# Kernel optimization log

Hardware: AMD Instinct MI355X
Metric: run time of the kernel (lower is better)

Reference implementation:

```python
import jax, jax.numpy as jnp
import numpy as np

N = 50000        # nodes
DEG = 16         # in-degree per node
E = N * DEG      # edges
IN_F, HID, NCLS = 128, 128, 64
B, L = 1024, 50  # sentence batch, sentence length


def _linear_init(key, fan_in, fan_out):
    s = 1.0 / np.sqrt(fan_in)
    kw, kb = jax.random.split(key)
    W = jax.random.uniform(kw, (fan_in, fan_out), jnp.float32, -s, s)
    b = jax.random.uniform(kb, (fan_out,), jnp.float32, -s, s)
    return W, b


def setup_inputs() -> dict:
    key = jax.random.key(0)
    ks = jax.random.split(key, 9)
    inputs = jax.random.normal(ks[0], (N, IN_F), jnp.float32)
    src = jax.random.randint(ks[1], (E,), 0, N, dtype=jnp.int32)
    # every node has exactly DEG incoming edges -> DGL recv on all nodes is well-defined
    dst = jnp.repeat(jnp.arange(N, dtype=jnp.int32), DEG)
    sentence = jax.random.randint(ks[2], (B, L), 0, N, dtype=jnp.int32)
    W1, b1 = _linear_init(ks[3], IN_F, HID)
    W2, b2 = _linear_init(ks[4], HID, NCLS)
    Wf1, bf1 = _linear_init(ks[5], NCLS, 256)
    Wf2, bf2 = _linear_init(ks[6], 256, 128)
    Wf3, bf3 = _linear_init(ks[7], 128, 2)
    return {"inputs": inputs, "W1": W1, "b1": b1, "W2": W2, "b2": b2,
            "Wf1": Wf1, "bf1": bf1, "Wf2": Wf2, "bf2": bf2, "Wf3": Wf3, "bf3": bf3,
            "src": src, "dst": dst, "sentence": sentence}


def reference(inputs, W1, b1, W2, b2, Wf1, bf1, Wf2, bf2, Wf3, bf3, src, dst, sentence):
    def mean_agg(h):
        # gather src features, segment-mean over destinations (gcn_message/gcn_reduce)
        s = jax.ops.segment_sum(h[src], dst, num_segments=N)       # [N, d]
        cnt = jax.ops.segment_sum(jnp.ones((E, 1), h.dtype), dst, num_segments=N)
        return s / jnp.maximum(cnt, 1.0)

    x = jax.nn.relu(mean_agg(inputs) @ W1 + b1)   # gc1 + relu (dropout = identity, eval mode)
    x = mean_agg(x) @ W2 + b2                      # gc2
    x = x.at[0].set(0.0)                           # x[0] = zeros
    sent_emd = jnp.sum(x[sentence], axis=1)        # [B, NCLS]
    h1 = jax.nn.relu(sent_emd @ Wf1 + bf1)
    h2 = jax.nn.relu(h1 @ Wf2 + bf2)
    return h2 @ Wf3 + bf3                          # [B, 2]
```

## Files before the change

### kernel.cpp

```cpp
#include <hip/hip_runtime.h>

#define NNODES 50000
#define DEG    16
#define NCLS   64
#define BSENT  1024
#define LSENT  50

typedef __attribute__((ext_vector_type(8))) short short8;
typedef __attribute__((ext_vector_type(4))) float f32x4;

__device__ __forceinline__ unsigned short f2bf(float f) {
    union { float f; unsigned u; } v; v.f = f;
    unsigned r = v.u + 0x7fffu + ((v.u >> 16) & 1u);
    return (unsigned short)(r >> 16);
}
__device__ __forceinline__ unsigned pack2bf(float a, float b) {
    return (unsigned)f2bf(a) | ((unsigned)f2bf(b) << 16);
}

__device__ __forceinline__ void prep_one(const float* W, unsigned short* Bp,
                                         int idx, int NOUT) {
    int j    = idx & 7;
    int lane = (idx >> 3) & 63;
    int rem  = idx >> 9;
    int ks   = rem & 3, c = rem >> 2;
    int k = ks * 32 + (lane >> 4) * 8 + j;
    int n = c * 16 + (lane & 15);
    Bp[idx] = f2bf(W[k * NOUT + n]);
}

__global__ void prep_both(const float* __restrict__ W1, unsigned short* __restrict__ B1p,
                          const float* __restrict__ W2, unsigned short* __restrict__ B2p) {
    int idx = blockIdx.x * 256 + threadIdx.x;
    if (idx < 128 * 128)                 prep_one(W1, B1p, idx, 128);
    else if (idx < 128 * 128 + 64 * 128) prep_one(W2, B2p, idx - 128 * 128, 64);
}

__global__ __launch_bounds__(256)
void gemm_mfma1(const float* __restrict__ X, const unsigned short* __restrict__ Bp,
                unsigned short* __restrict__ Y, int M) {
    __shared__ __align__(16) unsigned short As[64 * 128];
    __shared__ __align__(16) unsigned short Bs[128 * 128];
    const int tid  = threadIdx.x;
    const int wave = tid >> 6, lane = tid & 63;
    const int mbase = blockIdx.x * 64;

#pragma unroll
    for (int i = 0; i < 8; ++i) {
        int idx = tid + i * 256;
        int row = idx >> 5;
        int c4  = idx & 31;
        int grow = mbase + row;
        int w  = row >> 4;
        int ks = c4 >> 3;
        int ln = ((c4 >> 1) & 3) * 16 + (row & 15);
        int off = ((w * 4 + ks) * 64 + ln) * 8 + (c4 & 1) * 4;
        unsigned lo = 0, hi = 0;
        if (grow < M) {
            const float4 v = *(const float4*)&X[(size_t)grow * 128 + c4 * 4];
            lo = pack2bf(v.x, v.y);
            hi = pack2bf(v.z, v.w);
        }
        *(uint2*)&As[off] = make_uint2(lo, hi);
    }
#pragma unroll
    for (int i = 0; i < 8; ++i) {
        int idx = tid + i * 256;
        *(uint4*)&Bs[idx * 8] = *(const uint4*)&Bp[idx * 8];
    }
    __syncthreads();

    const short8* Af = (const short8*)As;
    const short8* Bf = (const short8*)Bs;
    short8 a[4];
#pragma unroll
    for (int ks = 0; ks < 4; ++ks) a[ks] = Af[(wave * 4 + ks) * 64 + lane];

    f32x4 acc[8] = {};
#pragma unroll
    for (int c = 0; c < 8; ++c)
#pragma unroll
        for (int ks = 0; ks < 4; ++ks)
            acc[c] = __builtin_amdgcn_mfma_f32_16x16x32_bf16(
                a[ks], Bf[(c * 4 + ks) * 64 + lane], acc[c], 0, 0, 0);

    const int col = lane & 15, rg = lane >> 4;
#pragma unroll
    for (int c = 0; c < 8; ++c)
#pragma unroll
        for (int r = 0; r < 4; ++r) {
            int grow = mbase + wave * 16 + rg * 4 + r;
            if (grow < M) Y[(size_t)grow * 128 + c * 16 + col] = f2bf(acc[c][r]);
        }
}

__global__ __launch_bounds__(256)
void agg_gemm(const unsigned short* __restrict__ Y1, const int* __restrict__ src,
              const float* __restrict__ b1, const unsigned short* __restrict__ B2p,
              unsigned short* __restrict__ Y2, int M) {
    __shared__ __align__(16) unsigned short As[64 * 128];
    __shared__ __align__(16) unsigned short Bs[64 * 128];
    __shared__ int s_idx[64 * DEG];
    const int tid  = threadIdx.x;
    const int wave = tid >> 6, lane = tid & 63;
    const int mbase = blockIdx.x * 64;

    {
        const long eb = (long)mbase * DEG;
        int e = tid;
#pragma unroll
        for (int i = 0; i < 4; ++i, e += 256)
            s_idx[e] = (eb + e < (long)NNODES * DEG) ? src[eb + e] : 0;
    }
#pragma unroll
    for (int i = 0; i < 4; ++i) {
        int idx = tid + i * 256;
        *(uint4*)&Bs[idx * 8] = *(const uint4*)&B2p[idx * 8];
    }
    __syncthreads();

    const int c8    = tid & 15;
    const int rbase = tid >> 4;
    const int ks    = c8 >> 2;
    const int lncol = (c8 & 3) * 16;
#pragma unroll
    for (int it = 0; it < 4; ++it) {
        const int row  = it * 16 + rbase;
        const int grow = mbase + row;
        float a0 = 0.f, a1 = 0.f, a2 = 0.f, a3 = 0.f;
        float a4 = 0.f, a5 = 0.f, a6 = 0.f, a7 = 0.f;
        if (grow < M) {
            const int* sp = &s_idx[row * DEG];
#pragma unroll
            for (int j = 0; j < DEG; ++j) {
                const uint4 v = *(const uint4*)&Y1[(size_t)sp[j] * 128 + c8 * 8];
                a0 += __uint_as_float(v.x << 16);
                a1 += __uint_as_float(v.x & 0xffff0000u);
                a2 += __uint_as_float(v.y << 16);
                a3 += __uint_as_float(v.y & 0xffff0000u);
                a4 += __uint_as_float(v.z << 16);
                a5 += __uint_as_float(v.z & 0xffff0000u);
                a6 += __uint_as_float(v.w << 16);
                a7 += __uint_as_float(v.w & 0xffff0000u);
            }
            const float s = 1.f / 16.f;
            const float4 bb0 = *(const float4*)&b1[c8 * 8];
            const float4 bb1 = *(const float4*)&b1[c8 * 8 + 4];
            a0 = fmaxf(a0 * s + bb0.x, 0.f);
            a1 = fmaxf(a1 * s + bb0.y, 0.f);
            a2 = fmaxf(a2 * s + bb0.z, 0.f);
            a3 = fmaxf(a3 * s + bb0.w, 0.f);
            a4 = fmaxf(a4 * s + bb1.x, 0.f);
            a5 = fmaxf(a5 * s + bb1.y, 0.f);
            a6 = fmaxf(a6 * s + bb1.z, 0.f);
            a7 = fmaxf(a7 * s + bb1.w, 0.f);
        }
        const int off = ((it * 4 + ks) * 64 + lncol + rbase) * 8;
        uint4 o;
        o.x = pack2bf(a0, a1);
        o.y = pack2bf(a2, a3);
        o.z = pack2bf(a4, a5);
        o.w = pack2bf(a6, a7);
        *(uint4*)&As[off] = o;
    }
    __syncthreads();

    const short8* Af = (const short8*)As;
    const short8* Bf = (const short8*)Bs;
    short8 a[4];
#pragma unroll
    for (int ks2 = 0; ks2 < 4; ++ks2) a[ks2] = Af[(wave * 4 + ks2) * 64 + lane];

    f32x4 acc[4] = {};
#pragma unroll
    for (int c = 0; c < 4; ++c)
#pragma unroll
        for (int ks2 = 0; ks2 < 4; ++ks2)
            acc[c] = __builtin_amdgcn_mfma_f32_16x16x32_bf16(
                a[ks2], Bf[(c * 4 + ks2) * 64 + lane], acc[c], 0, 0, 0);

    const int col = lane & 15, rg = lane >> 4;
#pragma unroll
    for (int c = 0; c < 4; ++c)
#pragma unroll
        for (int r = 0; r < 4; ++r) {
            int grow = mbase + wave * 16 + rg * 4 + r;
            if (grow < M) Y2[(size_t)grow * 64 + c * 16 + col] = f2bf(acc[c][r]);
        }
}

__global__ __launch_bounds__(256)
void agg2(const unsigned short* __restrict__ Y, const int* __restrict__ src,
          const float* __restrict__ bias, float* __restrict__ out, int M) {
    __shared__ int s_idx[32 * DEG];
    const int tid = threadIdx.x;
    const int nb = blockIdx.x * 32;
    {
        const long eb = (long)nb * DEG;
        int e = tid;
#pragma unroll
        for (int i = 0; i < 2; ++i, e += 256)
            s_idx[e] = (eb + e < (long)NNODES * DEG) ? src[eb + e] : 0;
    }
    __syncthreads();
    const int row = tid >> 3, c8 = tid & 7;
    const int n = nb + row;
    if (n >= M) return;
    const int* sp = &s_idx[row * DEG];
    float a0 = 0.f, a1 = 0.f, a2 = 0.f, a3 = 0.f;
    float a4 = 0.f, a5 = 0.f, a6 = 0.f, a7 = 0.f;
#pragma unroll
    for (int j = 0; j < DEG; ++j) {
        const uint4 v = *(const uint4*)&Y[(size_t)sp[j] * 64 + c8 * 8];
        a0 += __uint_as_float(v.x << 16);
        a1 += __uint_as_float(v.x & 0xffff0000u);
        a2 += __uint_as_float(v.y << 16);
        a3 += __uint_as_float(v.y & 0xffff0000u);
        a4 += __uint_as_float(v.z << 16);
        a5 += __uint_as_float(v.z & 0xffff0000u);
        a6 += __uint_as_float(v.w << 16);
        a7 += __uint_as_float(v.w & 0xffff0000u);
    }
    const float s = 1.f / 16.f;
    const float4 b0 = *(const float4*)&bias[c8 * 8];
    const float4 b1v = *(const float4*)&bias[c8 * 8 + 4];
    a0 = a0 * s + b0.x;  a1 = a1 * s + b0.y;
    a2 = a2 * s + b0.z;  a3 = a3 * s + b0.w;
    a4 = a4 * s + b1v.x; a5 = a5 * s + b1v.y;
    a6 = a6 * s + b1v.z; a7 = a7 * s + b1v.w;
    if (n == 0) { a0 = a1 = a2 = a3 = a4 = a5 = a6 = a7 = 0.f; }
    float* op = &out[(size_t)n * 64 + c8 * 8];
    *(float4*)op       = make_float4(a0, a1, a2, a3);
    *(float4*)(op + 4) = make_float4(a4, a5, a6, a7);
}

__global__ __launch_bounds__(256)
void head_fused(const float* __restrict__ x2, const int* __restrict__ sentence,
                const float* __restrict__ Wf1, const float* __restrict__ bf1,
                const float* __restrict__ Wf2, const float* __restrict__ bf2,
                const float* __restrict__ Wf3, const float* __restrict__ bf3,
                float* __restrict__ out) {
    __shared__ int   s_idx[8 * LSENT];
    __shared__ float sent_s[8][64];
    __shared__ float h1_s[8][256];
    __shared__ float h2_s[8][128];
    const int tid = threadIdx.x;
    const int bs = blockIdx.x * 8;

    for (int e = tid; e < 8 * LSENT; e += 256)
        s_idx[e] = sentence[bs * LSENT + e];
    __syncthreads();

    {
        const int s = tid >> 5, l32 = tid & 31;
        float c0 = 0.f, c1 = 0.f;
        const int* sp = &s_idx[s * LSENT];
#pragma unroll 5
        for (int l = 0; l < LSENT; ++l) {
            const float2 v = *(const float2*)&x2[(size_t)sp[l] * 64 + l32 * 2];
            c0 += v.x; c1 += v.y;
        }
        sent_s[s][l32 * 2 + 0] = c0;
        sent_s[s][l32 * 2 + 1] = c1;
    }
    __syncthreads();

    {
        const int s = tid >> 5, og = (tid & 31) * 8;
        float acc[8];
#pragma unroll
        for (int j = 0; j < 8; ++j) acc[j] = bf1[og + j];
        for (int k = 0; k < 64; ++k) {
            const float xk = sent_s[s][k];
            const float4 w0 = *(const float4*)&Wf1[k * 256 + og];
            const float4 w1 = *(const float4*)&Wf1[k * 256 + og + 4];
            acc[0] += xk * w0.x; acc[1] += xk * w0.y; acc[2] += xk * w0.z; acc[3] += xk * w0.w;
            acc[4] += xk * w1.x; acc[5] += xk * w1.y; acc[6] += xk * w1.z; acc[7] += xk * w1.w;
        }
#pragma unroll
        for (int j = 0; j < 8; ++j) h1_s[s][og + j] = fmaxf(acc[j], 0.f);
    }
    __syncthreads();

    {
        const int s = tid >> 5, og = (tid & 31) * 4;
        float acc[4];
#pragma unroll
        for (int j = 0; j < 4; ++j) acc[j] = bf2[og + j];
        for (int k = 0; k < 256; ++k) {
            const float xk = h1_s[s][k];
            const float4 w = *(const float4*)&Wf2[k * 128 + og];
            acc[0] += xk * w.x; acc[1] += xk * w.y; acc[2] += xk * w.z; acc[3] += xk * w.w;
        }
#pragma unroll
        for (int j = 0; j < 4; ++j) h2_s[s][og + j] = fmaxf(acc[j], 0.f);
    }
    __syncthreads();

    if (tid < 16) {
        const int s = tid >> 1, c = tid & 1;
        float acc = bf3[c];
        for (int k = 0; k < 128; ++k)
            acc += h2_s[s][k] * Wf3[k * 2 + c];
        out[(bs + s) * 2 + c] = acc;
    }
}

extern "C" void kernel_launch(void* const* d_in, const int* in_sizes, int n_in,
                              void* d_out, int out_size, void* d_ws, size_t ws_size,
                              hipStream_t stream) {
    const float* inputs  = (const float*)d_in[0];
    const float* W1      = (const float*)d_in[1];
    const float* b1      = (const float*)d_in[2];
    const float* W2      = (const float*)d_in[3];
    const float* b2      = (const float*)d_in[4];
    const float* Wf1     = (const float*)d_in[5];
    const float* bf1     = (const float*)d_in[6];
    const float* Wf2     = (const float*)d_in[7];
    const float* bf2     = (const float*)d_in[8];
    const float* Wf3     = (const float*)d_in[9];
    const float* bf3     = (const float*)d_in[10];
    const int*   src     = (const int*)d_in[11];
    const int*   sentence= (const int*)d_in[13];
    float* out = (float*)d_out;

    char* ws = (char*)d_ws;
    size_t o = 0;
    auto alloc = [&](size_t bytes) -> char* {
        char* p = ws + o; o += (bytes + 255) & ~(size_t)255; return p;
    };
    unsigned short* Y1  = (unsigned short*)alloc((size_t)NNODES * 128 * 2);
    unsigned short* Y2  = (unsigned short*)alloc((size_t)NNODES * 64 * 2);
    float*          x2  = (float*)alloc((size_t)NNODES * 64 * 4);
    unsigned short* B1p = (unsigned short*)alloc(128 * 128 * 2);
    unsigned short* B2p = (unsigned short*)alloc(64 * 128 * 2);

    const int gridM = (NNODES + 63) / 64;

    prep_both<<<(128 * 128 + 64 * 128 + 255) / 256, 256, 0, stream>>>(W1, B1p, W2, B2p);
    gemm_mfma1<<<gridM, 256, 0, stream>>>(inputs, B1p, Y1, NNODES);
    agg_gemm<<<gridM, 256, 0, stream>>>(Y1, src, b1, B2p, Y2, NNODES);
    agg2<<<(NNODES + 31) / 32, 256, 0, stream>>>(Y2, src, b2, x2, NNODES);
    head_fused<<<BSENT / 8, 256, 0, stream>>>(x2, sentence, Wf1, bf1, Wf2, bf2, Wf3, bf3, out);
}
```

Baseline: 90.43 us.

## Fuse weight bf16 conversion into GEMM kernels and narrow aggregation gather

Removes the separate prep kernel that converted W1/W2 into the MFMA bf16 fragment layout. Each GEMM block now reads the fp32 weights and converts and scatters them into shared memory itself, which saves one launch but repeats the conversion in every one of the roughly 782 blocks and adds scalar LDS stores. The first-layer aggregation in agg_gemm also changes from 16-byte gathers covering 8 features per thread to 8-byte gathers covering 4 features, looping 8 times per thread, which reuses the A-tile store layout from gemm_mfma1. Index arithmetic is switched from long to int.

```diff
diff --git a/kernel.cpp b/kernel.cpp
--- a/kernel.cpp
+++ b/kernel.cpp
@@ -18,26 +18,25 @@
     return (unsigned)f2bf(a) | ((unsigned)f2bf(b) << 16);
 }
 
-__device__ __forceinline__ void prep_one(const float* W, unsigned short* Bp,
-                                         int idx, int NOUT) {
-    int j    = idx & 7;
-    int lane = (idx >> 3) & 63;
-    int rem  = idx >> 9;
-    int ks   = rem & 3, c = rem >> 2;
-    int k = ks * 32 + (lane >> 4) * 8 + j;
-    int n = c * 16 + (lane & 15);
-    Bp[idx] = f2bf(W[k * NOUT + n]);
-}
-
-__global__ void prep_both(const float* __restrict__ W1, unsigned short* __restrict__ B1p,
-                          const float* __restrict__ W2, unsigned short* __restrict__ B2p) {
-    int idx = blockIdx.x * 256 + threadIdx.x;
-    if (idx < 128 * 128)                 prep_one(W1, B1p, idx, 128);
-    else if (idx < 128 * 128 + 64 * 128) prep_one(W2, B2p, idx - 128 * 128, 64);
+template<int NOUT>
+__device__ __forceinline__ void stage_B(const float* __restrict__ W,
+                                        unsigned short* Bs, int tid) {
+#pragma unroll
+    for (int i = 0; i < 128 * NOUT / (256 * 4); ++i) {
+        const int e4 = (tid + i * 256) * 4;
+        const int k = e4 / NOUT, n = e4 % NOUT;
+        const float4 w = *(const float4*)&W[e4];
+        const int g16 = ((k >> 3) & 3) * 16;
+        const int base = (((n >> 4) * 4 + (k >> 5)) * 64 + g16 + (n & 15)) * 8 + (k & 7);
+        Bs[base]      = f2bf(w.x);
+        Bs[base + 8]  = f2bf(w.y);
+        Bs[base + 16] = f2bf(w.z);
+        Bs[base + 24] = f2bf(w.w);
+    }
 }
 
 __global__ __launch_bounds__(256)
-void gemm_mfma1(const float* __restrict__ X, const unsigned short* __restrict__ Bp,
+void gemm_mfma1(const float* __restrict__ X, const float* __restrict__ W1,
                 unsigned short* __restrict__ Y, int M) {
     __shared__ __align__(16) unsigned short As[64 * 128];
     __shared__ __align__(16) unsigned short Bs[128 * 128];
@@ -45,16 +44,16 @@
     const int wave = tid >> 6, lane = tid & 63;
     const int mbase = blockIdx.x * 64;
 
+    stage_B<128>(W1, Bs, tid);
+
 #pragma unroll
     for (int i = 0; i < 8; ++i) {
         int idx = tid + i * 256;
         int row = idx >> 5;
         int c4  = idx & 31;
         int grow = mbase + row;
-        int w  = row >> 4;
-        int ks = c4 >> 3;
-        int ln = ((c4 >> 1) & 3) * 16 + (row & 15);
-        int off = ((w * 4 + ks) * 64 + ln) * 8 + (c4 & 1) * 4;
+        int off = (((row >> 4) * 4 + (c4 >> 3)) * 64 +
+                   ((c4 >> 1) & 3) * 16 + (row & 15)) * 8 + (c4 & 1) * 4;
         unsigned lo = 0, hi = 0;
         if (grow < M) {
             const float4 v = *(const float4*)&X[(size_t)grow * 128 + c4 * 4];
@@ -63,11 +62,6 @@
         }
         *(uint2*)&As[off] = make_uint2(lo, hi);
     }
-#pragma unroll
-    for (int i = 0; i < 8; ++i) {
-        int idx = tid + i * 256;
-        *(uint4*)&Bs[idx * 8] = *(const uint4*)&Bp[idx * 8];
-    }
     __syncthreads();
 
     const short8* Af = (const short8*)As;
@@ -96,7 +90,7 @@
 
 __global__ __launch_bounds__(256)
 void agg_gemm(const unsigned short* __restrict__ Y1, const int* __restrict__ src,
-              const float* __restrict__ b1, const unsigned short* __restrict__ B2p,
+              const float* __restrict__ b1, const float* __restrict__ W2,
               unsigned short* __restrict__ Y2, int M) {
     __shared__ __align__(16) unsigned short As[64 * 128];
     __shared__ __align__(16) unsigned short Bs[64 * 128];
@@ -105,63 +99,42 @@
     const int wave = tid >> 6, lane = tid & 63;
     const int mbase = blockIdx.x * 64;
 
-    {
-        const long eb = (long)mbase * DEG;
+    stage_B<64>(W2, Bs, tid);
+    {
+        const int eb = mbase * DEG;
         int e = tid;
 #pragma unroll
         for (int i = 0; i < 4; ++i, e += 256)
-            s_idx[e] = (eb + e < (long)NNODES * DEG) ? src[eb + e] : 0;
-    }
-#pragma unroll
-    for (int i = 0; i < 4; ++i) {
-        int idx = tid + i * 256;
-        *(uint4*)&Bs[idx * 8] = *(const uint4*)&B2p[idx * 8];
-    }
-    __syncthreads();
-
-    const int c8    = tid & 15;
-    const int rbase = tid >> 4;
-    const int ks    = c8 >> 2;
-    const int lncol = (c8 & 3) * 16;
-#pragma unroll
-    for (int it = 0; it < 4; ++it) {
-        const int row  = it * 16 + rbase;
-        const int grow = mbase + row;
+            s_idx[e] = (eb + e < NNODES * DEG) ? src[eb + e] : 0;
+    }
+    __syncthreads();
+
+#pragma unroll
+    for (int i = 0; i < 8; ++i) {
+        int slot = tid + i * 256;
+        int row = slot >> 5, c4 = slot & 31;
+        int grow = mbase + row;
         float a0 = 0.f, a1 = 0.f, a2 = 0.f, a3 = 0.f;
-        float a4 = 0.f, a5 = 0.f, a6 = 0.f, a7 = 0.f;
         if (grow < M) {
             const int* sp = &s_idx[row * DEG];
 #pragma unroll
             for (int j = 0; j < DEG; ++j) {
-                const uint4 v = *(const uint4*)&Y1[(size_t)sp[j] * 128 + c8 * 8];
+                const uint2 v = *(const uint2*)&Y1[(size_t)sp[j] * 128 + c4 * 4];
                 a0 += __uint_as_float(v.x << 16);
                 a1 += __uint_as_float(v.x & 0xffff0000u);
                 a2 += __uint_as_float(v.y << 16);
                 a3 += __uint_as_float(v.y & 0xffff0000u);
-                a4 += __uint_as_float(v.z << 16);
-                a5 += __uint_as_float(v.z & 0xffff0000u);
-                a6 += __uint_as_float(v.w << 16);
-                a7 += __uint_as_float(v.w & 0xffff0000u);
             }
             const float s = 1.f / 16.f;
-            const float4 bb0 = *(const float4*)&b1[c8 * 8];
-            const float4 bb1 = *(const float4*)&b1[c8 * 8 + 4];
-            a0 = fmaxf(a0 * s + bb0.x, 0.f);
-            a1 = fmaxf(a1 * s + bb0.y, 0.f);
-            a2 = fmaxf(a2 * s + bb0.z, 0.f);
-            a3 = fmaxf(a3 * s + bb0.w, 0.f);
-            a4 = fmaxf(a4 * s + bb1.x, 0.f);
-            a5 = fmaxf(a5 * s + bb1.y, 0.f);
-            a6 = fmaxf(a6 * s + bb1.z, 0.f);
-            a7 = fmaxf(a7 * s + bb1.w, 0.f);
-        }
-        const int off = ((it * 4 + ks) * 64 + lncol + rbase) * 8;
-        uint4 o;
-        o.x = pack2bf(a0, a1);
-        o.y = pack2bf(a2, a3);
-        o.z = pack2bf(a4, a5);
-        o.w = pack2bf(a6, a7);
-        *(uint4*)&As[off] = o;
+            const float4 bb = *(const float4*)&b1[c4 * 4];
+            a0 = fmaxf(a0 * s + bb.x, 0.f);
+            a1 = fmaxf(a1 * s + bb.y, 0.f);
+            a2 = fmaxf(a2 * s + bb.z, 0.f);
+            a3 = fmaxf(a3 * s + bb.w, 0.f);
+        }
+        int off = (((row >> 4) * 4 + (c4 >> 3)) * 64 +
+                   ((c4 >> 1) & 3) * 16 + (row & 15)) * 8 + (c4 & 1) * 4;
+        *(uint2*)&As[off] = make_uint2(pack2bf(a0, a1), pack2bf(a2, a3));
     }
     __syncthreads();
 
@@ -169,15 +142,15 @@
     const short8* Bf = (const short8*)Bs;
     short8 a[4];
 #pragma unroll
-    for (int ks2 = 0; ks2 < 4; ++ks2) a[ks2] = Af[(wave * 4 + ks2) * 64 + lane];
+    for (int ks = 0; ks < 4; ++ks) a[ks] = Af[(wave * 4 + ks) * 64 + lane];
 
     f32x4 acc[4] = {};
 #pragma unroll
     for (int c = 0; c < 4; ++c)
 #pragma unroll
-        for (int ks2 = 0; ks2 < 4; ++ks2)
+        for (int ks = 0; ks < 4; ++ks)
             acc[c] = __builtin_amdgcn_mfma_f32_16x16x32_bf16(
-                a[ks2], Bf[(c * 4 + ks2) * 64 + lane], acc[c], 0, 0, 0);
+                a[ks], Bf[(c * 4 + ks) * 64 + lane], acc[c], 0, 0, 0);
 
     const int col = lane & 15, rg = lane >> 4;
 #pragma unroll
@@ -196,11 +169,11 @@
     const int tid = threadIdx.x;
     const int nb = blockIdx.x * 32;
     {
-        const long eb = (long)nb * DEG;
+        const int eb = nb * DEG;
         int e = tid;
 #pragma unroll
         for (int i = 0; i < 2; ++i, e += 256)
-            s_idx[e] = (eb + e < (long)NNODES * DEG) ? src[eb + e] : 0;
+            s_idx[e] = (eb + e < NNODES * DEG) ? src[eb + e] : 0;
     }
     __syncthreads();
     const int row = tid >> 3, c8 = tid & 7;
@@ -329,17 +302,14 @@
     auto alloc = [&](size_t bytes) -> char* {
         char* p = ws + o; o += (bytes + 255) & ~(size_t)255; return p;
     };
-    unsigned short* Y1  = (unsigned short*)alloc((size_t)NNODES * 128 * 2);
-    unsigned short* Y2  = (unsigned short*)alloc((size_t)NNODES * 64 * 2);
-    float*          x2  = (float*)alloc((size_t)NNODES * 64 * 4);
-    unsigned short* B1p = (unsigned short*)alloc(128 * 128 * 2);
-    unsigned short* B2p = (unsigned short*)alloc(64 * 128 * 2);
+    unsigned short* Y1 = (unsigned short*)alloc((size_t)NNODES * 128 * 2);
+    unsigned short* Y2 = (unsigned short*)alloc((size_t)NNODES * 64 * 2);
+    float*          x2 = (float*)alloc((size_t)NNODES * 64 * 4);
 
     const int gridM = (NNODES + 63) / 64;
 
-    prep_both<<<(128 * 128 + 64 * 128 + 255) / 256, 256, 0, stream>>>(W1, B1p, W2, B2p);
-    gemm_mfma1<<<gridM, 256, 0, stream>>>(inputs, B1p, Y1, NNODES);
-    agg_gemm<<<gridM, 256, 0, stream>>>(Y1, src, b1, B2p, Y2, NNODES);
+    gemm_mfma1<<<gridM, 256, 0, stream>>>(inputs, W1, Y1, NNODES);
+    agg_gemm<<<gridM, 256, 0, stream>>>(Y1, src, b1, W2, Y2, NNODES);
     agg2<<<(NNODES + 31) / 32, 256, 0, stream>>>(Y2, src, b2, x2, NNODES);
     head_fused<<<BSENT / 8, 256, 0, stream>>>(x2, sentence, Wf1, bf1, Wf2, bf2, Wf3, bf3, out);
 }
```

After: 97.13 us. 7.4% more time.
